# Optimization experiments

Hardware: AMD Instinct MI355X
Metric: run time of the kernel (lower is better)

The kernel has to match this reference:

```python
import jax, jax.numpy as jnp
import numpy as np

N_DRUG = 572
EMB = 256
K_NB = 128
N_TAIL = 100000
N_REL = 200
N_EDGE = 4576
BN_EPS = 1e-5


def setup_inputs() -> dict:
    key = jax.random.key(0)
    ks = jax.random.split(key, 12)
    return {
        "drug_name": jnp.arange(N_DRUG, dtype=jnp.int64 if jax.config.jax_enable_x64 else jnp.int32),
        "adj_tail": jax.random.randint(ks[0], (N_DRUG, K_NB), 0, N_TAIL),
        "adj_relation": jax.random.randint(ks[1], (N_DRUG, K_NB), 0, N_REL),
        "nb_src": jax.random.randint(ks[2], (N_EDGE,), 0, N_DRUG),
        "nb_dst": jax.random.randint(ks[3], (N_EDGE,), 0, N_DRUG),
        "epoch": 2,
        # learned parameters
        "drug_table": jax.random.normal(ks[4], (N_DRUG, EMB), dtype=jnp.float32),
        "rela_table": jax.random.normal(ks[5], (N_REL, EMB), dtype=jnp.float32),
        "ent_table": jax.random.normal(ks[6], (N_TAIL, EMB), dtype=jnp.float32),
        "lin_W": jax.random.normal(ks[7], (2 * EMB, EMB), dtype=jnp.float32) * (1.0 / np.sqrt(2 * EMB)),
        "lin_b": jnp.zeros((EMB,), dtype=jnp.float32),
        "bn_gamma": jnp.ones((EMB,), dtype=jnp.float32),
        "bn_beta": jnp.zeros((EMB,), dtype=jnp.float32),
    }


def reference(drug_name, adj_tail, adj_relation, nb_src, nb_dst, epoch,
              drug_table, rela_table, ent_table, lin_W, lin_b, bn_gamma, bn_beta):
    # --- embedding gathers ---
    d = drug_table[drug_name]          # [N, E]
    r = rela_table[adj_relation]       # [N, K, E]
    e = ent_table[adj_tail]            # [N, K, E]

    # --- attention over sampled neighbors (KGNN-style: score = <drug, relation>) ---
    scores = jnp.einsum('ne,nke->nk', d, r)              # [N, K]
    alpha = jax.nn.softmax(scores, axis=1)               # softmax over neighbors
    attended = jnp.einsum('nk,nke->ne', alpha, e)        # [N, E]

    # --- Linear(2E -> E) + ReLU + BatchNorm1d (training-mode batch stats) ---
    x = jnp.concatenate([attended, d], axis=1)           # [N, 2E]
    h = jax.nn.relu(x @ lin_W + lin_b)                   # [N, E]
    mean = jnp.mean(h, axis=0)
    var = jnp.mean((h - mean) ** 2, axis=0)              # biased var, as in torch BN
    drug_f = (h - mean) * jax.lax.rsqrt(var + BN_EPS) * bn_gamma + bn_beta

    # --- invariant-adjacency segment-average scatter update (epoch > 1) ---
    if epoch > 1:
        nb_sum = jax.ops.segment_sum(drug_f[nb_src], nb_dst, num_segments=N_DRUG)   # [N, E]
        cnt = jax.ops.segment_sum(jnp.ones_like(nb_dst, dtype=drug_f.dtype), nb_dst,
                                  num_segments=N_DRUG)                               # [N]
        nb_avg = nb_sum / jnp.maximum(cnt, 1.0)[:, None]
        drug_f = jnp.where((cnt > 0)[:, None], (nb_avg + drug_f) * 0.5, drug_f)
    return drug_f
```

## Files before the change

### kernel.cpp

```cpp
#include <hip/hip_runtime.h>

#define N_DRUG 572
#define EMB    256
#define K_NB   128
#define N_EDGE 4576
#define BN_EPS 1e-5f

__global__ __launch_bounds__(256) void scores_kernel(
    const int* __restrict__ drug_name,
    const int* __restrict__ adj_relation,
    const float* __restrict__ drug_table,
    const float* __restrict__ rela_table,
    float* __restrict__ alphas)
{
    __shared__ float ld[EMB];
    __shared__ float sc[K_NB];
    __shared__ float wred[2];

    const int b    = blockIdx.x;
    const int tid  = threadIdx.x;
    const int lane = tid & 63;
    const int wv   = tid >> 6;

    ld[tid] = drug_table[(size_t)drug_name[b] * EMB + tid];
    __syncthreads();

    const float4 dv = ((const float4*)ld)[lane];
    for (int k = wv; k < K_NB; k += 4) {
        const int rel = adj_relation[b * K_NB + k];
        const float4 rv = ((const float4*)(rela_table + (size_t)rel * EMB))[lane];
        float p = dv.x * rv.x + dv.y * rv.y + dv.z * rv.z + dv.w * rv.w;
        #pragma unroll
        for (int off = 32; off > 0; off >>= 1)
            p += __shfl_xor(p, off, 64);
        if (lane == 0) sc[k] = p;
    }
    __syncthreads();

    float pv = 0.f;
    if (tid < K_NB) {
        float m = sc[tid];
        #pragma unroll
        for (int off = 32; off > 0; off >>= 1)
            m = fmaxf(m, __shfl_xor(m, off, 64));
        if (lane == 0) wred[wv] = m;
    }
    __syncthreads();
    if (tid < K_NB) {
        const float m = fmaxf(wred[0], wred[1]);
        pv = __expf(sc[tid] - m);
        float s = pv;
        #pragma unroll
        for (int off = 32; off > 0; off >>= 1)
            s += __shfl_xor(s, off, 64);
        if (lane == 0) wred[wv] = s;
    }
    __syncthreads();
    if (tid < K_NB) {
        const float tot = wred[0] + wred[1];
        alphas[(size_t)b * K_NB + tid] = pv / tot;
    }
}

#define NCHUNK 4
#define CK (K_NB / NCHUNK)
__global__ __launch_bounds__(256) void gather_kernel(
    const int* __restrict__ adj_tail,
    const float* __restrict__ alphas,
    const float* __restrict__ ent_table,
    float* __restrict__ att)
{
    __shared__ float part[4][EMB];

    const int b    = blockIdx.x / NCHUNK;
    const int c    = blockIdx.x % NCHUNK;
    const int tid  = threadIdx.x;
    const int lane = tid & 63;
    const int wv   = tid >> 6;

    const int base = b * K_NB + c * CK + wv * 8;
    float4 acc = make_float4(0.f, 0.f, 0.f, 0.f);
    #pragma unroll
    for (int j = 0; j < 8; ++j) {
        const float a = alphas[base + j];
        const int   t = adj_tail[base + j];
        const float4 ev = ((const float4*)(ent_table + (size_t)t * EMB))[lane];
        acc.x = fmaf(a, ev.x, acc.x);
        acc.y = fmaf(a, ev.y, acc.y);
        acc.z = fmaf(a, ev.z, acc.z);
        acc.w = fmaf(a, ev.w, acc.w);
    }
    ((float4*)part[wv])[lane] = acc;
    __syncthreads();
    const float v = part[0][tid] + part[1][tid] + part[2][tid] + part[3][tid];
    atomicAdd(&att[(size_t)b * EMB + tid], v);
}

__global__ __launch_bounds__(512) void linear_kernel(
    const int* __restrict__ drug_name,
    const float* __restrict__ att,
    const float* __restrict__ drug_table,
    const float* __restrict__ lin_W,
    const float* __restrict__ lin_b,
    float* __restrict__ h,
    float* __restrict__ s1,
    float* __restrict__ s2)
{
    __shared__ float xs[2 * EMB];
    __shared__ float part[2][EMB];

    const int b   = blockIdx.x;
    const int tid = threadIdx.x;

    if (tid < EMB) xs[tid] = att[(size_t)b * EMB + tid];
    else           xs[tid] = drug_table[(size_t)drug_name[b] * EMB + (tid - EMB)];
    __syncthreads();

    const int col  = tid & (EMB - 1);
    const int half = tid >> 8;
    const float* wp = lin_W + (size_t)(half * EMB) * EMB + col;
    const float* xp = xs + half * EMB;
    float acc = 0.f;
    #pragma unroll 8
    for (int i = 0; i < EMB; ++i)
        acc = fmaf(xp[i], wp[(size_t)i * EMB], acc);
    part[half][col] = acc;
    __syncthreads();

    if (tid < EMB) {
        const float v = fmaxf(part[0][tid] + part[1][tid] + lin_b[tid], 0.f);
        h[(size_t)b * EMB + tid] = v;
        atomicAdd(&s1[tid], v);
        atomicAdd(&s2[tid], v * v);
    }
}

#define EPB 8
__global__ __launch_bounds__(256) void scatter_bn(
    const int* __restrict__ nb_src, const int* __restrict__ nb_dst,
    const int* __restrict__ epoch,
    const float* __restrict__ h,
    const float* __restrict__ s1, const float* __restrict__ s2,
    const float* __restrict__ gamma, const float* __restrict__ beta,
    float* __restrict__ nb_sum,
    float* __restrict__ cnt)
{
    if (*epoch <= 1) return;
    const int tid = threadIdx.x;
    const float invN  = 1.0f / (float)N_DRUG;
    const float mean  = s1[tid] * invN;
    const float var   = s2[tid] * invN - mean * mean;
    const float scale = gamma[tid] * rsqrtf(var + BN_EPS);
    const float bet   = beta[tid];

    const int e0 = blockIdx.x * EPB;
    const int e1 = min(e0 + EPB, N_EDGE);
    for (int e = e0; e < e1; ++e) {
        const int s = nb_src[e];
        const int d = nb_dst[e];
        const float f = (h[(size_t)s * EMB + tid] - mean) * scale + bet;
        atomicAdd(&nb_sum[(size_t)d * EMB + tid], f);
        if (tid == 0) atomicAdd(&cnt[d], 1.0f);
    }
}

__global__ __launch_bounds__(256) void combine_bn(
    const float* __restrict__ h,
    const float* __restrict__ s1, const float* __restrict__ s2,
    const float* __restrict__ gamma, const float* __restrict__ beta,
    const float* __restrict__ nb_sum,
    const float* __restrict__ cnt,
    const int* __restrict__ epoch,
    float* __restrict__ out)
{
    const int b   = blockIdx.x;
    const int tid = threadIdx.x;
    const size_t idx = (size_t)b * EMB + tid;
    const float invN  = 1.0f / (float)N_DRUG;
    const float mean  = s1[tid] * invN;
    const float var   = s2[tid] * invN - mean * mean;
    const float scale = gamma[tid] * rsqrtf(var + BN_EPS);
    float f = (h[idx] - mean) * scale + beta[tid];
    if (*epoch > 1) {
        const float c = cnt[b];
        if (c > 0.f) f = (nb_sum[idx] / c + f) * 0.5f;
    }
    out[idx] = f;
}

extern "C" void kernel_launch(void* const* d_in, const int* in_sizes, int n_in,
                              void* d_out, int out_size, void* d_ws, size_t ws_size,
                              hipStream_t stream) {
    const int*   drug_name    = (const int*)d_in[0];
    const int*   adj_tail     = (const int*)d_in[1];
    const int*   adj_relation = (const int*)d_in[2];
    const int*   nb_src       = (const int*)d_in[3];
    const int*   nb_dst       = (const int*)d_in[4];
    const int*   epoch        = (const int*)d_in[5];
    const float* drug_table   = (const float*)d_in[6];
    const float* rela_table   = (const float*)d_in[7];
    const float* ent_table    = (const float*)d_in[8];
    const float* lin_W        = (const float*)d_in[9];
    const float* lin_b        = (const float*)d_in[10];
    const float* bn_gamma     = (const float*)d_in[11];
    const float* bn_beta      = (const float*)d_in[12];
    float* out = (float*)d_out;

    float* ws = (float*)d_ws;
    float* h      = ws;
    float* s1     = h + N_DRUG * EMB;
    float* s2     = s1 + EMB;
    float* cnt    = s2 + EMB;
    float* nb_sum = cnt + N_DRUG;
    float* att    = nb_sum + N_DRUG * EMB;
    float* alphas = att + N_DRUG * EMB;
    const size_t zero_bytes =
        (size_t)(EMB + EMB + N_DRUG + 2 * N_DRUG * EMB) * sizeof(float);

    hipMemsetAsync(s1, 0, zero_bytes, stream);

    scores_kernel<<<N_DRUG, 256, 0, stream>>>(drug_name, adj_relation,
                                              drug_table, rela_table, alphas);

    gather_kernel<<<N_DRUG * NCHUNK, 256, 0, stream>>>(adj_tail, alphas,
                                                       ent_table, att);

    linear_kernel<<<N_DRUG, 512, 0, stream>>>(drug_name, att, drug_table,
                                              lin_W, lin_b, h, s1, s2);

    scatter_bn<<<(N_EDGE + EPB - 1) / EPB, 256, 0, stream>>>(nb_src, nb_dst, epoch,
                                                             h, s1, s2, bn_gamma, bn_beta,
                                                             nb_sum, cnt);

    combine_bn<<<N_DRUG, 256, 0, stream>>>(h, s1, s2, bn_gamma, bn_beta,
                                           nb_sum, cnt, epoch, out);
}
```

Before: 232.1 us.

## Split score kernel across chunks and move softmax into gather kernel

The score computation now runs over four times as many blocks, each computing 32 relation dot products with eight independent loads in flight per wave, and writes raw scores. Softmax normalization moves into the gather kernel, which each chunk block recomputes redundantly from the 128 scores in shared memory. The linear kernel unroll goes from 8 to 16, and scatter_bn processes 2 edges per block instead of 8, giving more blocks and dropping the bounds check. The cost is redundant softmax work in every gather block, plus more atomic-heavy blocks in the scatter.

```diff
diff --git a/kernel.cpp b/kernel.cpp
--- a/kernel.cpp
+++ b/kernel.cpp
@@ -5,36 +5,60 @@
 #define K_NB   128
 #define N_EDGE 4576
 #define BN_EPS 1e-5f
-
-__global__ __launch_bounds__(256) void scores_kernel(
+#define NCHUNK 4
+
+__global__ __launch_bounds__(256) void scores2_kernel(
     const int* __restrict__ drug_name,
     const int* __restrict__ adj_relation,
     const float* __restrict__ drug_table,
     const float* __restrict__ rela_table,
-    float* __restrict__ alphas)
-{
-    __shared__ float ld[EMB];
-    __shared__ float sc[K_NB];
-    __shared__ float wred[2];
-
-    const int b    = blockIdx.x;
+    float* __restrict__ scores)
+{
+    const int b    = blockIdx.x / NCHUNK;
+    const int c    = blockIdx.x % NCHUNK;
     const int tid  = threadIdx.x;
     const int lane = tid & 63;
     const int wv   = tid >> 6;
 
-    ld[tid] = drug_table[(size_t)drug_name[b] * EMB + tid];
-    __syncthreads();
-
-    const float4 dv = ((const float4*)ld)[lane];
-    for (int k = wv; k < K_NB; k += 4) {
-        const int rel = adj_relation[b * K_NB + k];
-        const float4 rv = ((const float4*)(rela_table + (size_t)rel * EMB))[lane];
-        float p = dv.x * rv.x + dv.y * rv.y + dv.z * rv.z + dv.w * rv.w;
+    const float4 dv =
+        ((const float4*)(drug_table + (size_t)drug_name[b] * EMB))[lane];
+
+    const int kbase = c * 32 + wv * 8;
+    float p[8];
+    #pragma unroll
+    for (int j = 0; j < 8; ++j) {
+        const int rel = adj_relation[b * K_NB + kbase + j];
+        const float4 rv =
+            ((const float4*)(rela_table + (size_t)rel * EMB))[lane];
+        p[j] = dv.x * rv.x + dv.y * rv.y + dv.z * rv.z + dv.w * rv.w;
+    }
+    #pragma unroll
+    for (int j = 0; j < 8; ++j) {
+        float s = p[j];
         #pragma unroll
         for (int off = 32; off > 0; off >>= 1)
-            p += __shfl_xor(p, off, 64);
-        if (lane == 0) sc[k] = p;
-    }
+            s += __shfl_xor(s, off, 64);
+        if (lane == 0) scores[(size_t)b * K_NB + kbase + j] = s;
+    }
+}
+
+__global__ __launch_bounds__(256) void gather2_kernel(
+    const int* __restrict__ adj_tail,
+    const float* __restrict__ scores,
+    const float* __restrict__ ent_table,
+    float* __restrict__ att)
+{
+    __shared__ float sc[K_NB];
+    __shared__ float wred[2];
+    __shared__ float part[4][EMB];
+
+    const int b    = blockIdx.x / NCHUNK;
+    const int c    = blockIdx.x % NCHUNK;
+    const int tid  = threadIdx.x;
+    const int lane = tid & 63;
+    const int wv   = tid >> 6;
+
+    if (tid < K_NB) sc[tid] = scores[(size_t)b * K_NB + tid];
     __syncthreads();
 
     float pv = 0.f;
@@ -56,34 +80,16 @@
         if (lane == 0) wred[wv] = s;
     }
     __syncthreads();
-    if (tid < K_NB) {
-        const float tot = wred[0] + wred[1];
-        alphas[(size_t)b * K_NB + tid] = pv / tot;
-    }
-}
-
-#define NCHUNK 4
-#define CK (K_NB / NCHUNK)
-__global__ __launch_bounds__(256) void gather_kernel(
-    const int* __restrict__ adj_tail,
-    const float* __restrict__ alphas,
-    const float* __restrict__ ent_table,
-    float* __restrict__ att)
-{
-    __shared__ float part[4][EMB];
-
-    const int b    = blockIdx.x / NCHUNK;
-    const int c    = blockIdx.x % NCHUNK;
-    const int tid  = threadIdx.x;
-    const int lane = tid & 63;
-    const int wv   = tid >> 6;
-
-    const int base = b * K_NB + c * CK + wv * 8;
+    if (tid < K_NB) sc[tid] = pv / (wred[0] + wred[1]);
+    __syncthreads();
+
+    const int kbase = c * 32 + wv * 8;
     float4 acc = make_float4(0.f, 0.f, 0.f, 0.f);
     #pragma unroll
     for (int j = 0; j < 8; ++j) {
-        const float a = alphas[base + j];
-        const int   t = adj_tail[base + j];
+        const int k = kbase + j;
+        const float a = sc[k];
+        const int   t = adj_tail[b * K_NB + k];
         const float4 ev = ((const float4*)(ent_table + (size_t)t * EMB))[lane];
         acc.x = fmaf(a, ev.x, acc.x);
         acc.y = fmaf(a, ev.y, acc.y);
@@ -121,7 +127,7 @@
     const float* wp = lin_W + (size_t)(half * EMB) * EMB + col;
     const float* xp = xs + half * EMB;
     float acc = 0.f;
-    #pragma unroll 8
+    #pragma unroll 16
     for (int i = 0; i < EMB; ++i)
         acc = fmaf(xp[i], wp[(size_t)i * EMB], acc);
     part[half][col] = acc;
@@ -135,7 +141,7 @@
     }
 }
 
-#define EPB 8
+#define EPB 2
 __global__ __launch_bounds__(256) void scatter_bn(
     const int* __restrict__ nb_src, const int* __restrict__ nb_dst,
     const int* __restrict__ epoch,
@@ -154,8 +160,8 @@
     const float bet   = beta[tid];
 
     const int e0 = blockIdx.x * EPB;
-    const int e1 = min(e0 + EPB, N_EDGE);
-    for (int e = e0; e < e1; ++e) {
+    #pragma unroll
+    for (int e = e0; e < e0 + EPB; ++e) {
         const int s = nb_src[e];
         const int d = nb_dst[e];
         const float f = (h[(size_t)s * EMB + tid] - mean) * scale + bet;
@@ -213,24 +219,24 @@
     float* cnt    = s2 + EMB;
     float* nb_sum = cnt + N_DRUG;
     float* att    = nb_sum + N_DRUG * EMB;
-    float* alphas = att + N_DRUG * EMB;
+    float* scores = att + N_DRUG * EMB;
     const size_t zero_bytes =
         (size_t)(EMB + EMB + N_DRUG + 2 * N_DRUG * EMB) * sizeof(float);
 
     hipMemsetAsync(s1, 0, zero_bytes, stream);
 
-    scores_kernel<<<N_DRUG, 256, 0, stream>>>(drug_name, adj_relation,
-                                              drug_table, rela_table, alphas);
-
-    gather_kernel<<<N_DRUG * NCHUNK, 256, 0, stream>>>(adj_tail, alphas,
-                                                       ent_table, att);
+    scores2_kernel<<<N_DRUG * NCHUNK, 256, 0, stream>>>(drug_name, adj_relation,
+                                                        drug_table, rela_table, scores);
+
+    gather2_kernel<<<N_DRUG * NCHUNK, 256, 0, stream>>>(adj_tail, scores,
+                                                        ent_table, att);
 
     linear_kernel<<<N_DRUG, 512, 0, stream>>>(drug_name, att, drug_table,
                                               lin_W, lin_b, h, s1, s2);
 
-    scatter_bn<<<(N_EDGE + EPB - 1) / EPB, 256, 0, stream>>>(nb_src, nb_dst, epoch,
-                                                             h, s1, s2, bn_gamma, bn_beta,
-                                                             nb_sum, cnt);
+    scatter_bn<<<N_EDGE / EPB, 256, 0, stream>>>(nb_src, nb_dst, epoch,
+                                                 h, s1, s2, bn_gamma, bn_beta,
+                                                 nb_sum, cnt);
 
     combine_bn<<<N_DRUG, 256, 0, stream>>>(h, s1, s2, bn_gamma, bn_beta,
                                            nb_sum, cnt, epoch, out);
```

Result: faster. 220.9 us (-4.8%).
